# Performance work log

Hardware: AMD Instinct MI355X
Metric: run time of the kernel (lower is better)

Reference implementation:

```python
import jax, jax.numpy as jnp
import numpy as np
import math

N_LAYERS = 8
D = 1024
H = 16
DK = D // H
T = 1024
V = 32000
B = 2
DFF = 4 * D
EPS = 1e-5


def layernorm(x, scale, bias):
    mu = jnp.mean(x, axis=-1, keepdims=True)
    var = jnp.mean(jnp.square(x - mu), axis=-1, keepdims=True)
    return (x - mu) * jax.lax.rsqrt(var + EPS) * scale + bias


def setup_inputs() -> dict:
    key = jax.random.key(0)
    ks = jax.random.split(key, 32)
    s = 0.02
    rn = lambda k, shape: jax.random.normal(k, shape, dtype=jnp.float32) * s
    x = jax.random.randint(ks[0], (B, T), 0, V)
    return {
        "x": x,
        "inp_emb": rn(ks[1], (V, D)),
        "pos_emb": rn(ks[2], (T, D)),
        # per-layer weights stacked on leading layer axis; per-head wq/wk/wv are
        # concatenated along the output dim (mathematically identical to the
        # per-head nn.Linear list in the torch code)
        "wq": rn(ks[3], (N_LAYERS, D, D)), "bq": jnp.zeros((N_LAYERS, D), jnp.float32),
        "wk": rn(ks[4], (N_LAYERS, D, D)), "bk": jnp.zeros((N_LAYERS, D), jnp.float32),
        "wv": rn(ks[5], (N_LAYERS, D, D)), "bv": jnp.zeros((N_LAYERS, D), jnp.float32),
        "wo": rn(ks[6], (N_LAYERS, D, D)), "bo": jnp.zeros((N_LAYERS, D), jnp.float32),
        "w1": rn(ks[7], (N_LAYERS, D, DFF)), "b1": jnp.zeros((N_LAYERS, DFF), jnp.float32),
        "w2": rn(ks[8], (N_LAYERS, DFF, D)), "b2": jnp.zeros((N_LAYERS, D), jnp.float32),
        "ln1_s": jnp.ones((N_LAYERS, D), jnp.float32), "ln1_b": jnp.zeros((N_LAYERS, D), jnp.float32),
        "ln2_s": jnp.ones((N_LAYERS, D), jnp.float32), "ln2_b": jnp.zeros((N_LAYERS, D), jnp.float32),
        "lno_s": jnp.ones((D,), jnp.float32), "lno_b": jnp.zeros((D,), jnp.float32),
        "w_out": rn(ks[9], (D, V)),
    }


def reference(x, inp_emb, pos_emb, wq, bq, wk, bk, wv, bv, wo, bo,
              w1, b1, w2, b2, ln1_s, ln1_b, ln2_s, ln2_b, lno_s, lno_b, w_out):
    h = inp_emb[x] + pos_emb[jnp.arange(T)]            # [B,T,D]
    causal = jnp.tril(jnp.ones((T, T), dtype=bool))    # [T,T]
    scale = 1.0 / math.sqrt(DK)
    for i in range(N_LAYERS):
        # --- multi-head causal attention ---
        xn = layernorm(h, ln1_s[i], ln1_b[i])
        q = (xn @ wq[i] + bq[i]).reshape(B, T, H, DK)
        k = (xn @ wk[i] + bk[i]).reshape(B, T, H, DK)
        v = (xn @ wv[i] + bv[i]).reshape(B, T, H, DK)
        scores = jnp.einsum('bqhd,bkhd->bhqk', q, k) * scale
        scores = jnp.where(causal, scores, -jnp.inf)
        att = jax.nn.softmax(scores, axis=-1)           # [B,H,T,T]
        y = jnp.einsum('bhqk,bkhd->bqhd', att, v).reshape(B, T, D)
        h = h + y @ wo[i] + bo[i]
        # --- feed-forward ---
        xn = layernorm(h, ln2_s[i], ln2_b[i])
        h = h + jax.nn.gelu(xn @ w1[i] + b1[i], approximate=False) @ w2[i] + b2[i]
    h = layernorm(h, lno_s, lno_b)
    return h @ w_out                                    # logits [B,T,V]
```

## Files before the change

kernel.cpp:

```cpp
#include <hip/hip_runtime.h>
#include <cmath>

#define D_MODEL 1024
#define N_HEADS 16
#define DKH     64
#define SEQ_T   1024
#define BATCH   2
#define VOCAB   32000
#define DFF_    4096
#define NLAYERS 8

typedef __bf16 bf16x8 __attribute__((ext_vector_type(8)));
typedef __bf16 bf16x4v __attribute__((ext_vector_type(4)));
typedef float  f32x4  __attribute__((ext_vector_type(4)));

__device__ __forceinline__ float gelu_f(float x) {
    return 0.5f * x * (1.0f + erff(x * 0.70710678118654752f));
}

__device__ __forceinline__ void gload_lds16(const void* g, void* l) {
    __builtin_amdgcn_global_load_lds(
        (const __attribute__((address_space(1))) void*)g,
        (__attribute__((address_space(3))) void*)l, 16, 0, 0);
}

__global__ __launch_bounds__(256) void embed_kernel(
    const int* __restrict__ x, const float* __restrict__ inp_emb,
    const float* __restrict__ pos_emb, float* __restrict__ h)
{
    const int idx = blockIdx.x * 256 + threadIdx.x;
    const int bt  = idx >> 10;
    const int d   = idx & 1023;
    const int t   = bt & (SEQ_T - 1);
    const int tok = x[bt];
    h[idx] = inp_emb[(size_t)tok * D_MODEL + d] + pos_emb[(size_t)t * D_MODEL + d];
}

__device__ __forceinline__ void ln_row(
    const float* __restrict__ x, const float* __restrict__ sc,
    const float* __restrict__ bi, __bf16* __restrict__ o, int row, int tid)
{
    const int c = tid * 4;
    const float4 v = *(const float4*)(x + (size_t)row * D_MODEL + c);
    float sum = v.x + v.y + v.z + v.w;
    float sq  = v.x * v.x + v.y * v.y + v.z * v.z + v.w * v.w;
    #pragma unroll
    for (int off = 32; off > 0; off >>= 1) {
        sum += __shfl_xor(sum, off);
        sq  += __shfl_xor(sq, off);
    }
    __shared__ float ssum[4], ssq[4];
    const int wave = tid >> 6, lane = tid & 63;
    if (lane == 0) { ssum[wave] = sum; ssq[wave] = sq; }
    __syncthreads();
    sum = ssum[0] + ssum[1] + ssum[2] + ssum[3];
    sq  = ssq[0]  + ssq[1]  + ssq[2]  + ssq[3];
    const float mu  = sum * (1.0f / D_MODEL);
    const float var = sq * (1.0f / D_MODEL) - mu * mu;
    const float rs  = rsqrtf(var + 1e-5f);
    const float4 s4 = *(const float4*)(sc + c);
    const float4 b4 = *(const float4*)(bi + c);
    bf16x4v ov;
    ov[0] = (__bf16)((v.x - mu) * rs * s4.x + b4.x);
    ov[1] = (__bf16)((v.y - mu) * rs * s4.y + b4.y);
    ov[2] = (__bf16)((v.z - mu) * rs * s4.z + b4.z);
    ov[3] = (__bf16)((v.w - mu) * rs * s4.w + b4.w);
    *(bf16x4v*)(o + (size_t)row * D_MODEL + c) = ov;
}

__global__ __launch_bounds__(256) void layernorm_kernel(
    const float* __restrict__ x, const float* __restrict__ sc,
    const float* __restrict__ bi, __bf16* __restrict__ o)
{
    ln_row(x, sc, bi, o, blockIdx.x, threadIdx.x);
}

__global__ __launch_bounds__(256) void wout_tr_kernel(
    const float* __restrict__ in, __bf16* __restrict__ out)
{
    __shared__ __bf16 tile[32][72];
    const int tid = threadIdx.x;
    const int t   = blockIdx.x;
    const int kb0 = (t & 31) * 32;
    const int nb0 = (t >> 5) * 64;
    {
        const int rr = tid >> 3, c8 = (tid & 7) * 8;
        const float* p = in + (size_t)(kb0 + rr) * VOCAB + nb0 + c8;
        const float4 v0 = *(const float4*)p;
        const float4 v1 = *(const float4*)(p + 4);
        tile[rr][c8 + 0] = (__bf16)v0.x;
        tile[rr][c8 + 1] = (__bf16)v0.y;
        tile[rr][c8 + 2] = (__bf16)v0.z;
        tile[rr][c8 + 3] = (__bf16)v0.w;
        tile[rr][c8 + 4] = (__bf16)v1.x;
        tile[rr][c8 + 5] = (__bf16)v1.y;
        tile[rr][c8 + 6] = (__bf16)v1.z;
        tile[rr][c8 + 7] = (__bf16)v1.w;
    }
    __syncthreads();
    {
        const int cc = tid >> 2, k8 = (tid & 3) * 8;
        bf16x8 ov;
        #pragma unroll
        for (int e = 0; e < 8; ++e) ov[e] = tile[k8 + e][cc];
        *(bf16x8*)(out + (size_t)(nb0 + cc) * D_MODEL + kb0 + k8) = ov;
    }
}

__global__ __launch_bounds__(256) void prep_ln_kernel(
    const float* __restrict__ h, const float* __restrict__ ln_s,
    const float* __restrict__ ln_b, __bf16* __restrict__ xn,
    const float* __restrict__ wq, const float* __restrict__ wk,
    const float* __restrict__ wv, const float* __restrict__ wo,
    const float* __restrict__ w1, const float* __restrict__ w2,
    const float* __restrict__ bq, const float* __restrict__ bk,
    const float* __restrict__ bv,
    __bf16* __restrict__ wqkvT, __bf16* __restrict__ woT,
    __bf16* __restrict__ w1T, __bf16* __restrict__ w2T,
    float* __restrict__ bqkv)
{
    const int tid = threadIdx.x;
    const int b   = blockIdx.x;

    if (b < 2048) {
        ln_row(h, ln_s, ln_b, xn, b, tid);
        return;
    }
    const int pb = b - 2048;
    if (pb >= 6144) {
        const int j = (pb - 6144) * 256 + tid;
        bqkv[j] = (j < 1024) ? bq[j] : (j < 2048 ? bk[j - 1024] : bv[j - 2048]);
        return;
    }

    __shared__ __bf16 tile[32][72];
    const float* in;
    __bf16* out;
    int K, N, kb0, nb0;
    if (pb < 2048) {
        const int w = pb >> 9, t = pb & 511;
        K = 1024; N = 1024; kb0 = (t >> 4) * 32; nb0 = (t & 15) * 64;
        in  = (w == 0) ? wq : (w == 1) ? wk : (w == 2) ? wv : wo;
        out = (w == 3) ? woT : wqkvT + (size_t)w * 1024 * 1024;
    } else if (pb < 4096) {
        const int t = pb - 2048;
        K = 1024; N = 4096; kb0 = (t >> 6) * 32; nb0 = (t & 63) * 64;
        in = w1; out = w1T;
    } else {
        const int t = pb - 4096;
        K = 4096; N = 1024; kb0 = (t >> 4) * 32; nb0 = (t & 15) * 64;
        in = w2; out = w2T;
    }

    {
        const int rr = tid >> 3, c8 = (tid & 7) * 8;
        const float* p = in + (size_t)(kb0 + rr) * N + nb0 + c8;
        const float4 v0 = *(const float4*)p;
        const float4 v1 = *(const float4*)(p + 4);
        tile[rr][c8 + 0] = (__bf16)v0.x;
        tile[rr][c8 + 1] = (__bf16)v0.y;
        tile[rr][c8 + 2] = (__bf16)v0.z;
        tile[rr][c8 + 3] = (__bf16)v0.w;
        tile[rr][c8 + 4] = (__bf16)v1.x;
        tile[rr][c8 + 5] = (__bf16)v1.y;
        tile[rr][c8 + 6] = (__bf16)v1.z;
        tile[rr][c8 + 7] = (__bf16)v1.w;
    }
    __syncthreads();
    {
        const int cc = tid >> 2, k8 = (tid & 3) * 8;
        bf16x8 ov;
        #pragma unroll
        for (int e = 0; e < 8; ++e) ov[e] = tile[k8 + e][cc];
        *(bf16x8*)(out + (size_t)(nb0 + cc) * K + kb0 + k8) = ov;
    }
}

template <int BN_T, int EPI, typename OutT, bool NT = false>
__global__ __launch_bounds__(256) void gemm_bt(
    const __bf16* __restrict__ A, const __bf16* __restrict__ Bt,
    const float* __restrict__ bias, const float* __restrict__ res,
    OutT* __restrict__ C, int M, int N, int K)
{
    constexpr int NF  = BN_T / 32;
    constexpr int NCB = BN_T / 8;
    __shared__ __bf16 As[128 * 64];
    __shared__ __bf16 Bs[BN_T * 64];

    const int tid  = threadIdx.x;
    const int wave = tid >> 6;
    const int lane = tid & 63;
    const int r    = lane & 15;
    const int kb   = lane >> 4;
    const int wm   = wave >> 1;
    const int wn   = wave & 1;

    const int ntm = gridDim.x;
    const int nwg = ntm * gridDim.y;
    int bid = blockIdx.y * ntm + blockIdx.x;
    if ((nwg & 7) == 0) bid = (bid & 7) * (nwg >> 3) + (bid >> 3);
    const int bm = (bid % ntm) * 128;
    const int bn = (bid / ntm) * BN_T;

    const int srow = lane >> 3;
    const int sg   = lane & 7;

    f32x4 acc[4][NF] = {};

    for (int k0 = 0; k0 < K; k0 += 64) {
        #pragma unroll
        for (int i = 0; i < 4; ++i) {
            const int c    = i * 4 + wave;
            const int row  = c * 8 + srow;
            const int scol = (sg ^ (row & 7)) * 8;
            gload_lds16(A + (size_t)(bm + row) * K + k0 + scol, &As[c * 512]);
        }
        #pragma unroll
        for (int i = 0; i < NCB / 4; ++i) {
            const int c    = i * 4 + wave;
            const int row  = c * 8 + srow;
            const int scol = (sg ^ (row & 7)) * 8;
            gload_lds16(Bt + (size_t)(bn + row) * K + k0 + scol, &Bs[c * 512]);
        }
        __syncthreads();

        #pragma unroll
        for (int s = 0; s < 2; ++s) {
            bf16x8 af[4];
            #pragma unroll
            for (int m = 0; m < 4; ++m) {
                const int row = wm * 64 + m * 16 + r;
                const int g   = (s * 4 + kb) ^ (row & 7);
                af[m] = *(const bf16x8*)&As[row * 64 + g * 8];
            }
            #pragma unroll
            for (int n = 0; n < NF; ++n) {
                const int row = wn * (NF * 16) + n * 16 + r;
                const int g   = (s * 4 + kb) ^ (row & 7);
                const bf16x8 bfr = *(const bf16x8*)&Bs[row * 64 + g * 8];
                #pragma unroll
                for (int m = 0; m < 4; ++m)
                    acc[m][n] = __builtin_amdgcn_mfma_f32_16x16x32_bf16(af[m], bfr, acc[m][n], 0, 0, 0);
            }
        }
        __syncthreads();
    }

    #pragma unroll
    for (int m = 0; m < 4; ++m) {
        const int row = bm + wm * 64 + m * 16 + kb * 4;
        #pragma unroll
        for (int n = 0; n < NF; ++n) {
            const int col = bn + wn * (NF * 16) + n * 16 + r;
            const float bv = bias ? bias[col] : 0.0f;
            #pragma unroll
            for (int rg = 0; rg < 4; ++rg) {
                float v = acc[m][n][rg] + bv;
                if constexpr (EPI == 1) v += res[(size_t)(row + rg) * N + col];
                if constexpr (EPI == 2) v = gelu_f(v);
                if constexpr (NT) {
                    __builtin_nontemporal_store((OutT)v, &C[(size_t)(row + rg) * N + col]);
                } else {
                    C[(size_t)(row + rg) * N + col] = (OutT)v;
                }
            }
        }
    }
}

struct AttnState {
    float m[4];
    float l[4];
    f32x4 yacc[4];
};

template <bool MASK>
__device__ __forceinline__ void attn_tile_step(
    AttnState& st, const bf16x8 (&qf)[2], int q0, int kt,
    int wave, int r, int kb,
    const __bf16 (*K_lds)[72], const __bf16 (*V_lds)[72],
    __bf16 (*P_row)[72])
{
    f32x4 sacc[4] = {};
    #pragma unroll
    for (int kc = 0; kc < 2; ++kc) {
        #pragma unroll
        for (int g = 0; g < 4; ++g) {
            const bf16x8 kf = *(const bf16x8*)&K_lds[g * 16 + r][kc * 32 + kb * 8];
            sacc[g] = __builtin_amdgcn_mfma_f32_16x16x32_bf16(qf[kc], kf, sacc[g], 0, 0, 0);
        }
    }

    float s[4][4], p[4][4];
    #pragma unroll
    for (int g = 0; g < 4; ++g) {
        #pragma unroll
        for (int rg = 0; rg < 4; ++rg) {
            if constexpr (MASK) {
                const int key = kt * 64 + g * 16 + r;
                const int qq  = q0 + wave * 16 + kb * 4 + rg;
                s[g][rg] = (key <= qq) ? sacc[g][rg] * 0.125f : -INFINITY;
            } else {
                s[g][rg] = sacc[g][rg] * 0.125f;
            }
        }
    }

    float mt[4];
    #pragma unroll
    for (int rg = 0; rg < 4; ++rg)
        mt[rg] = fmaxf(fmaxf(s[0][rg], s[1][rg]), fmaxf(s[2][rg], s[3][rg]));
    #pragma unroll
    for (int off = 1; off < 16; off <<= 1) {
        #pragma unroll
        for (int rg = 0; rg < 4; ++rg) mt[rg] = fmaxf(mt[rg], __shfl_xor(mt[rg], off));
    }

    bool grow = false;
    #pragma unroll
    for (int rg = 0; rg < 4; ++rg) grow |= (mt[rg] > st.m[rg] + 8.0f);
    if (__any(grow)) {
        #pragma unroll
        for (int rg = 0; rg < 4; ++rg) {
            const float mn   = fmaxf(st.m[rg], mt[rg]);
            const float corr = __expf(st.m[rg] - mn);
            st.l[rg] *= corr;
            st.m[rg]  = mn;
            #pragma unroll
            for (int n = 0; n < 4; ++n) st.yacc[n][rg] *= corr;
        }
    }

    float psum[4];
    #pragma unroll
    for (int rg = 0; rg < 4; ++rg) {
        psum[rg] = 0.0f;
        #pragma unroll
        for (int g = 0; g < 4; ++g) {
            p[g][rg] = __expf(s[g][rg] - st.m[rg]);
            psum[rg] += p[g][rg];
        }
    }
    #pragma unroll
    for (int off = 1; off < 16; off <<= 1) {
        #pragma unroll
        for (int rg = 0; rg < 4; ++rg) psum[rg] += __shfl_xor(psum[rg], off);
    }
    #pragma unroll
    for (int rg = 0; rg < 4; ++rg) st.l[rg] += psum[rg];

    #pragma unroll
    for (int g = 0; g < 4; ++g) {
        #pragma unroll
        for (int rg = 0; rg < 4; ++rg)
            P_row[kb * 4 + rg][g * 16 + r] = (__bf16)p[g][rg];
    }
    const bf16x8 pa0 = *(const bf16x8*)&P_row[r][kb * 8];
    const bf16x8 pa1 = *(const bf16x8*)&P_row[r][32 + kb * 8];

    #pragma unroll
    for (int n = 0; n < 4; ++n) {
        const int vrow = n * 16 + r;
        const int swz  = (vrow >> 3) & 7;
        const bf16x8 vf0 = *(const bf16x8*)&V_lds[vrow][(kb ^ swz) * 8];
        st.yacc[n] = __builtin_amdgcn_mfma_f32_16x16x32_bf16(pa0, vf0, st.yacc[n], 0, 0, 0);
    }
    #pragma unroll
    for (int n = 0; n < 4; ++n) {
        const int vrow = n * 16 + r;
        const int swz  = (vrow >> 3) & 7;
        const bf16x8 vf1 = *(const bf16x8*)&V_lds[vrow][((kb + 4) ^ swz) * 8];
        st.yacc[n] = __builtin_amdgcn_mfma_f32_16x16x32_bf16(pa1, vf1, st.yacc[n], 0, 0, 0);
    }
}

__global__ __launch_bounds__(256) void attn_mfma_kernel(
    const __bf16* __restrict__ qkv, __bf16* __restrict__ y)
{
    constexpr int QS = 3 * D_MODEL;
    __shared__ __align__(16) __bf16 K_lds[64][72];
    __shared__ __align__(16) __bf16 V_lds[64][72];
    __shared__ __align__(16) __bf16 P_lds[4][16][72];

    const int tid  = threadIdx.x;
    const int wave = tid >> 6;
    const int lane = tid & 63;
    const int r    = lane & 15;
    const int kb   = lane >> 4;

    const int ip  = blockIdx.x;
    const int q0A = ip * 64;
    const int q0B = (15 - ip) * 64;
    const int b   = blockIdx.y >> 4;
    const int h   = blockIdx.y & 15;

    const __bf16* qp = qkv + (size_t)b * SEQ_T * QS + h * DKH;
    const __bf16* kp = qp + D_MODEL;
    const __bf16* vp = qp + 2 * D_MODEL;
    __bf16* yp = y + (size_t)b * SEQ_T * D_MODEL + h * DKH;

    bf16x8 qfA[2], qfB[2];
    {
        const int qrA = q0A + wave * 16 + r;
        const int qrB = q0B + wave * 16 + r;
        #pragma unroll
        for (int kc = 0; kc < 2; ++kc) {
            qfA[kc] = *(const bf16x8*)(qp + (size_t)qrA * QS + kc * 32 + kb * 8);
            qfB[kc] = *(const bf16x8*)(qp + (size_t)qrB * QS + kc * 32 + kb * 8);
        }
    }

    AttnState stA, stB;
    #pragma unroll
    for (int rg = 0; rg < 4; ++rg) {
        stA.m[rg] = -INFINITY; stA.l[rg] = 0.0f;
        stB.m[rg] = -INFINITY; stB.l[rg] = 0.0f;
    }
    #pragma unroll
    for (int n = 0; n < 4; ++n) { stA.yacc[n] = {}; stB.yacc[n] = {}; }

    const int skey = tid >> 2;
    const int sg16 = (tid & 3) * 16;
    const int swz0 = ((sg16 >> 3) & 7) * 8;
    const int swz1 = (((sg16 + 8) >> 3) & 7) * 8;

    const int ntiles = 16 - ip;

    bf16x8 kr0, kr1, vr0, vr1;
    {
        const size_t go = (size_t)skey * QS;
        kr0 = *(const bf16x8*)(kp + go + sg16);
        kr1 = *(const bf16x8*)(kp + go + sg16 + 8);
        vr0 = *(const bf16x8*)(vp + go + sg16);
        vr1 = *(const bf16x8*)(vp + go + sg16 + 8);
    }

    for (int kt = 0; kt < ntiles; ++kt) {
        *(bf16x8*)&K_lds[skey][sg16]     = kr0;
        *(bf16x8*)&K_lds[skey][sg16 + 8] = kr1;
        #pragma unroll
        for (int j = 0; j < 8; ++j)
            V_lds[sg16 + j][skey ^ swz0] = vr0[j];
        #pragma unroll
        for (int j = 0; j < 8; ++j)
            V_lds[sg16 + 8 + j][skey ^ swz1] = vr1[j];
        __syncthreads();

        if (kt + 1 < ntiles) {
            const size_t go = (size_t)((kt + 1) * 64 + skey) * QS;
            kr0 = *(const bf16x8*)(kp + go + sg16);
            kr1 = *(const bf16x8*)(kp + go + sg16 + 8);
            vr0 = *(const bf16x8*)(vp + go + sg16);
            vr1 = *(const bf16x8*)(vp + go + sg16 + 8);
        }

        if (kt == ntiles - 1)
            attn_tile_step<true >(stB, qfB, q0B, kt, wave, r, kb, K_lds, V_lds, P_lds[wave]);
        else
            attn_tile_step<false>(stB, qfB, q0B, kt, wave, r, kb, K_lds, V_lds, P_lds[wave]);
        if (kt <= ip) {
            if (kt == ip)
                attn_tile_step<true >(stA, qfA, q0A, kt, wave, r, kb, K_lds, V_lds, P_lds[wave]);
            else
                attn_tile_step<false>(stA, qfA, q0A, kt, wave, r, kb, K_lds, V_lds, P_lds[wave]);
        }
        __syncthreads();
    }

    float invA[4], invB[4];
    #pragma unroll
    for (int rg = 0; rg < 4; ++rg) {
        invA[rg] = 1.0f / stA.l[rg];
        invB[rg] = 1.0f / stB.l[rg];
    }
    #pragma unroll
    for (int n = 0; n < 4; ++n) {
        #pragma unroll
        for (int rg = 0; rg < 4; ++rg) {
            const int rowA = q0A + wave * 16 + kb * 4 + rg;
            const int rowB = q0B + wave * 16 + kb * 4 + rg;
            yp[(size_t)rowA * D_MODEL + n * 16 + r] = (__bf16)(stA.yacc[n][rg] * invA[rg]);
            yp[(size_t)rowB * D_MODEL + n * 16 + r] = (__bf16)(stB.yacc[n][rg] * invB[rg]);
        }
    }
}

extern "C" void kernel_launch(void* const* d_in, const int* in_sizes, int n_in,
                              void* d_out, int out_size, void* d_ws, size_t ws_size,
                              hipStream_t stream)
{
    const int*   x       = (const int*)  d_in[0];
    const float* inp_emb = (const float*)d_in[1];
    const float* pos_emb = (const float*)d_in[2];
    const float* wq = (const float*)d_in[3];
    const float* bq = (const float*)d_in[4];
    const float* wk = (const float*)d_in[5];
    const float* bk = (const float*)d_in[6];
    const float* wv = (const float*)d_in[7];
    const float* bv = (const float*)d_in[8];
    const float* wo = (const float*)d_in[9];
    const float* bo = (const float*)d_in[10];
    const float* w1 = (const float*)d_in[11];
    const float* b1 = (const float*)d_in[12];
    const float* w2 = (const float*)d_in[13];
    const float* b2 = (const float*)d_in[14];
    const float* ln1_s = (const float*)d_in[15];
    const float* ln1_b = (const float*)d_in[16];
    const float* ln2_s = (const float*)d_in[17];
    const float* ln2_b = (const float*)d_in[18];
    const float* lno_s = (const float*)d_in[19];
    const float* lno_b = (const float*)d_in[20];
    const float* w_out = (const float*)d_in[21];

    const int M = BATCH * SEQ_T;
    const size_t MB = 1u << 20;

    char* w = (char*)d_ws;
    float*  h     = (float*) (w + 0);
    __bf16* xn    = (__bf16*)(w + 8  * MB);
    __bf16* yb    = (__bf16*)(w + 12 * MB);
    __bf16* sh    = (__bf16*)(w + 16 * MB);
    __bf16* wqkvT = (__bf16*)(w + 32 * MB);
    __bf16* woT   = (__bf16*)(w + 38 * MB);
    __bf16* w1T   = (__bf16*)(w + 40 * MB);
    __bf16* w2T   = (__bf16*)(w + 48 * MB);
    float*  bqkv  = (float*) (w + 56 * MB);
    __bf16* woutT = (__bf16*)(w + 57 * MB);

    embed_kernel<<<dim3(M * D_MODEL / 256), 256, 0, stream>>>(x, inp_emb, pos_emb, h);

    for (int i = 0; i < NLAYERS; ++i) {
        const size_t wOff  = (size_t)i * D_MODEL * D_MODEL;
        const size_t w1Off = (size_t)i * D_MODEL * DFF_;

        prep_ln_kernel<<<dim3(2048 + 6156), 256, 0, stream>>>(
            h, ln1_s + i * D_MODEL, ln1_b + i * D_MODEL, xn,
            wq + wOff, wk + wOff, wv + wOff, wo + wOff, w1 + w1Off, w2 + w1Off,
            bq + i * D_MODEL, bk + i * D_MODEL, bv + i * D_MODEL,
            wqkvT, woT, w1T, w2T, bqkv);

        gemm_bt<64, 0, __bf16><<<dim3(M / 128, 3 * D_MODEL / 64), 256, 0, stream>>>(
            xn, wqkvT, bqkv, nullptr, sh, M, 3 * D_MODEL, D_MODEL);
        attn_mfma_kernel<<<dim3(8, BATCH * N_HEADS), 256, 0, stream>>>(sh, yb);
        gemm_bt<64, 1, float><<<dim3(M / 128, D_MODEL / 64), 256, 0, stream>>>(
            yb, woT, bo + i * D_MODEL, h, h, M, D_MODEL, D_MODEL);
        layernorm_kernel<<<dim3(M), 256, 0, stream>>>(h, ln2_s + i * D_MODEL, ln2_b + i * D_MODEL, xn);
        gemm_bt<128, 2, __bf16><<<dim3(M / 128, DFF_ / 128), 256, 0, stream>>>(
            xn, w1T, b1 + i * DFF_, nullptr, sh, M, DFF_, D_MODEL);
        gemm_bt<64, 1, float><<<dim3(M / 128, D_MODEL / 64), 256, 0, stream>>>(
            sh, w2T, b2 + i * D_MODEL, h, h, M, D_MODEL, DFF_);
    }

    wout_tr_kernel<<<dim3(16000), 256, 0, stream>>>(w_out, woutT);
    layernorm_kernel<<<dim3(M), 256, 0, stream>>>(h, lno_s, lno_b, xn);
    gemm_bt<128, 0, float, true><<<dim3(M / 128, VOCAB / 128), 256, 0, stream>>>(
        xn, woutT, nullptr, nullptr, (float*)d_out, M, VOCAB, D_MODEL);
}
```

Baseline: 1.631 ms.

## Store residual stream in bf16, double-buffer attention K/V, fuse final LN

```diff
diff --git a/kernel.cpp b/kernel.cpp
--- a/kernel.cpp
+++ b/kernel.cpp
@@ -26,24 +26,32 @@
 
 __global__ __launch_bounds__(256) void embed_kernel(
     const int* __restrict__ x, const float* __restrict__ inp_emb,
-    const float* __restrict__ pos_emb, float* __restrict__ h)
-{
-    const int idx = blockIdx.x * 256 + threadIdx.x;
+    const float* __restrict__ pos_emb, __bf16* __restrict__ h)
+{
+    const int idx = (blockIdx.x * 256 + threadIdx.x) * 4;
     const int bt  = idx >> 10;
     const int d   = idx & 1023;
     const int t   = bt & (SEQ_T - 1);
     const int tok = x[bt];
-    h[idx] = inp_emb[(size_t)tok * D_MODEL + d] + pos_emb[(size_t)t * D_MODEL + d];
+    const float4 a = *(const float4*)(inp_emb + (size_t)tok * D_MODEL + d);
+    const float4 b = *(const float4*)(pos_emb + (size_t)t * D_MODEL + d);
+    bf16x4v o;
+    o[0] = (__bf16)(a.x + b.x);
+    o[1] = (__bf16)(a.y + b.y);
+    o[2] = (__bf16)(a.z + b.z);
+    o[3] = (__bf16)(a.w + b.w);
+    *(bf16x4v*)(h + idx) = o;
 }
 
 __device__ __forceinline__ void ln_row(
-    const float* __restrict__ x, const float* __restrict__ sc,
+    const __bf16* __restrict__ x, const float* __restrict__ sc,
     const float* __restrict__ bi, __bf16* __restrict__ o, int row, int tid)
 {
     const int c = tid * 4;
-    const float4 v = *(const float4*)(x + (size_t)row * D_MODEL + c);
-    float sum = v.x + v.y + v.z + v.w;
-    float sq  = v.x * v.x + v.y * v.y + v.z * v.z + v.w * v.w;
+    const bf16x4v v4 = *(const bf16x4v*)(x + (size_t)row * D_MODEL + c);
+    const float vx = (float)v4[0], vy = (float)v4[1], vz = (float)v4[2], vw = (float)v4[3];
+    float sum = vx + vy + vz + vw;
+    float sq  = vx * vx + vy * vy + vz * vz + vw * vw;
     #pragma unroll
     for (int off = 32; off > 0; off >>= 1) {
         sum += __shfl_xor(sum, off);
@@ -61,25 +69,31 @@
     const float4 s4 = *(const float4*)(sc + c);
     const float4 b4 = *(const float4*)(bi + c);
     bf16x4v ov;
-    ov[0] = (__bf16)((v.x - mu) * rs * s4.x + b4.x);
-    ov[1] = (__bf16)((v.y - mu) * rs * s4.y + b4.y);
-    ov[2] = (__bf16)((v.z - mu) * rs * s4.z + b4.z);
-    ov[3] = (__bf16)((v.w - mu) * rs * s4.w + b4.w);
+    ov[0] = (__bf16)((vx - mu) * rs * s4.x + b4.x);
+    ov[1] = (__bf16)((vy - mu) * rs * s4.y + b4.y);
+    ov[2] = (__bf16)((vz - mu) * rs * s4.z + b4.z);
+    ov[3] = (__bf16)((vw - mu) * rs * s4.w + b4.w);
     *(bf16x4v*)(o + (size_t)row * D_MODEL + c) = ov;
 }
 
 __global__ __launch_bounds__(256) void layernorm_kernel(
-    const float* __restrict__ x, const float* __restrict__ sc,
+    const __bf16* __restrict__ x, const float* __restrict__ sc,
     const float* __restrict__ bi, __bf16* __restrict__ o)
 {
     ln_row(x, sc, bi, o, blockIdx.x, threadIdx.x);
 }
 
-__global__ __launch_bounds__(256) void wout_tr_kernel(
-    const float* __restrict__ in, __bf16* __restrict__ out)
-{
+__global__ __launch_bounds__(256) void wout_ln_kernel(
+    const float* __restrict__ in, __bf16* __restrict__ out,
+    const __bf16* __restrict__ h, const float* __restrict__ lno_s,
+    const float* __restrict__ lno_b, __bf16* __restrict__ xn)
+{
+    const int tid = threadIdx.x;
+    if (blockIdx.x >= 16000) {
+        ln_row(h, lno_s, lno_b, xn, blockIdx.x - 16000, tid);
+        return;
+    }
     __shared__ __bf16 tile[32][72];
-    const int tid = threadIdx.x;
     const int t   = blockIdx.x;
     const int kb0 = (t & 31) * 32;
     const int nb0 = (t >> 5) * 64;
@@ -108,7 +122,7 @@
 }
 
 __global__ __launch_bounds__(256) void prep_ln_kernel(
-    const float* __restrict__ h, const float* __restrict__ ln_s,
+    const __bf16* __restrict__ h, const float* __restrict__ ln_s,
     const float* __restrict__ ln_b, __bf16* __restrict__ xn,
     const float* __restrict__ wq, const float* __restrict__ wk,
     const float* __restrict__ wv, const float* __restrict__ wo,
@@ -179,7 +193,7 @@
 template <int BN_T, int EPI, typename OutT, bool NT = false>
 __global__ __launch_bounds__(256) void gemm_bt(
     const __bf16* __restrict__ A, const __bf16* __restrict__ Bt,
-    const float* __restrict__ bias, const float* __restrict__ res,
+    const float* __restrict__ bias, const OutT* __restrict__ res,
     OutT* __restrict__ C, int M, int N, int K)
 {
     constexpr int NF  = BN_T / 32;
@@ -256,7 +270,7 @@
             #pragma unroll
             for (int rg = 0; rg < 4; ++rg) {
                 float v = acc[m][n][rg] + bv;
-                if constexpr (EPI == 1) v += res[(size_t)(row + rg) * N + col];
+                if constexpr (EPI == 1) v += (float)res[(size_t)(row + rg) * N + col];
                 if constexpr (EPI == 2) v = gelu_f(v);
                 if constexpr (NT) {
                     __builtin_nontemporal_store((OutT)v, &C[(size_t)(row + rg) * N + col]);
@@ -378,8 +392,8 @@
     const __bf16* __restrict__ qkv, __bf16* __restrict__ y)
 {
     constexpr int QS = 3 * D_MODEL;
-    __shared__ __align__(16) __bf16 K_lds[64][72];
-    __shared__ __align__(16) __bf16 V_lds[64][72];
+    __shared__ __align__(16) __bf16 K_lds[2][64][72];
+    __shared__ __align__(16) __bf16 V_lds[2][64][72];
     __shared__ __align__(16) __bf16 P_lds[4][16][72];
 
     const int tid  = threadIdx.x;
@@ -434,19 +448,18 @@
         vr0 = *(const bf16x8*)(vp + go + sg16);
         vr1 = *(const bf16x8*)(vp + go + sg16 + 8);
     }
-
+    *(bf16x8*)&K_lds[0][skey][sg16]     = kr0;
+    *(bf16x8*)&K_lds[0][skey][sg16 + 8] = kr1;
+    #pragma unroll
+    for (int j = 0; j < 8; ++j) V_lds[0][sg16 + j][skey ^ swz0]     = vr0[j];
+    #pragma unroll
+    for (int j = 0; j < 8; ++j) V_lds[0][sg16 + 8 + j][skey ^ swz1] = vr1[j];
+    __syncthreads();
+
+    int cur = 0;
     for (int kt = 0; kt < ntiles; ++kt) {
-        *(bf16x8*)&K_lds[skey][sg16]     = kr0;
-        *(bf16x8*)&K_lds[skey][sg16 + 8] = kr1;
-        #pragma unroll
-        for (int j = 0; j < 8; ++j)
-            V_lds[sg16 + j][skey ^ swz0] = vr0[j];
-        #pragma unroll
-        for (int j = 0; j < 8; ++j)
-            V_lds[sg16 + 8 + j][skey ^ swz1] = vr1[j];
-        __syncthreads();
-
-        if (kt + 1 < ntiles) {
+        const bool has_next = (kt + 1 < ntiles);
+        if (has_next) {
             const size_t go = (size_t)((kt + 1) * 64 + skey) * QS;
             kr0 = *(const bf16x8*)(kp + go + sg16);
             kr1 = *(const bf16x8*)(kp + go + sg16 + 8);
@@ -455,16 +468,27 @@
         }
 
         if (kt == ntiles - 1)
-            attn_tile_step<true >(stB, qfB, q0B, kt, wave, r, kb, K_lds, V_lds, P_lds[wave]);
+            attn_tile_step<true >(stB, qfB, q0B, kt, wave, r, kb, K_lds[cur], V_lds[cur], P_lds[wave]);
         else
-            attn_tile_step<false>(stB, qfB, q0B, kt, wave, r, kb, K_lds, V_lds, P_lds[wave]);
+            attn_tile_step<false>(stB, qfB, q0B, kt, wave, r, kb, K_lds[cur], V_lds[cur], P_lds[wave]);
         if (kt <= ip) {
             if (kt == ip)
-                attn_tile_step<true >(stA, qfA, q0A, kt, wave, r, kb, K_lds, V_lds, P_lds[wave]);
+                attn_tile_step<true >(stA, qfA, q0A, kt, wave, r, kb, K_lds[cur], V_lds[cur], P_lds[wave]);
             else
-                attn_tile_step<false>(stA, qfA, q0A, kt, wave, r, kb, K_lds, V_lds, P_lds[wave]);
+                attn_tile_step<false>(stA, qfA, q0A, kt, wave, r, kb, K_lds[cur], V_lds[cur], P_lds[wave]);
+        }
+
+        if (has_next) {
+            const int nb = cur ^ 1;
+            *(bf16x8*)&K_lds[nb][skey][sg16]     = kr0;
+            *(bf16x8*)&K_lds[nb][skey][sg16 + 8] = kr1;
+            #pragma unroll
+            for (int j = 0; j < 8; ++j) V_lds[nb][sg16 + j][skey ^ swz0]     = vr0[j];
+            #pragma unroll
+            for (int j = 0; j < 8; ++j) V_lds[nb][sg16 + 8 + j][skey ^ swz1] = vr1[j];
         }
         __syncthreads();
+        cur ^= 1;
     }
 
     float invA[4], invB[4];
@@ -516,7 +540,7 @@
     const size_t MB = 1u << 20;
 
     char* w = (char*)d_ws;
-    float*  h     = (float*) (w + 0);
+    __bf16* h     = (__bf16*)(w + 0);
     __bf16* xn    = (__bf16*)(w + 8  * MB);
     __bf16* yb    = (__bf16*)(w + 12 * MB);
     __bf16* sh    = (__bf16*)(w + 16 * MB);
@@ -527,7 +551,7 @@
     float*  bqkv  = (float*) (w + 56 * MB);
     __bf16* woutT = (__bf16*)(w + 57 * MB);
 
-    embed_kernel<<<dim3(M * D_MODEL / 256), 256, 0, stream>>>(x, inp_emb, pos_emb, h);
+    embed_kernel<<<dim3(M * D_MODEL / 1024), 256, 0, stream>>>(x, inp_emb, pos_emb, h);
 
     for (int i = 0; i < NLAYERS; ++i) {
         const size_t wOff  = (size_t)i * D_MODEL * D_MODEL;
@@ -542,17 +566,17 @@
         gemm_bt<64, 0, __bf16><<<dim3(M / 128, 3 * D_MODEL / 64), 256, 0, stream>>>(
             xn, wqkvT, bqkv, nullptr, sh, M, 3 * D_MODEL, D_MODEL);
         attn_mfma_kernel<<<dim3(8, BATCH * N_HEADS), 256, 0, stream>>>(sh, yb);
-        gemm_bt<64, 1, float><<<dim3(M / 128, D_MODEL / 64), 256, 0, stream>>>(
+        gemm_bt<64, 1, __bf16><<<dim3(M / 128, D_MODEL / 64), 256, 0, stream>>>(
             yb, woT, bo + i * D_MODEL, h, h, M, D_MODEL, D_MODEL);
         layernorm_kernel<<<dim3(M), 256, 0, stream>>>(h, ln2_s + i * D_MODEL, ln2_b + i * D_MODEL, xn);
         gemm_bt<128, 2, __bf16><<<dim3(M / 128, DFF_ / 128), 256, 0, stream>>>(
             xn, w1T, b1 + i * DFF_, nullptr, sh, M, DFF_, D_MODEL);
-        gemm_bt<64, 1, float><<<dim3(M / 128, D_MODEL / 64), 256, 0, stream>>>(
+        gemm_bt<64, 1, __bf16><<<dim3(M / 128, D_MODEL / 64), 256, 0, stream>>>(
             sh, w2T, b2 + i * D_MODEL, h, h, M, D_MODEL, DFF_);
     }
 
-    wout_tr_kernel<<<dim3(16000), 256, 0, stream>>>(w_out, woutT);
-    layernorm_kernel<<<dim3(M), 256, 0, stream>>>(h, lno_s, lno_b, xn);
+    wout_ln_kernel<<<dim3(16000 + 2048), 256, 0, stream>>>(
+        w_out, woutT, h, lno_s, lno_b, xn);
     gemm_bt<128, 0, float, true><<<dim3(M / 128, VOCAB / 128), 256, 0, stream>>>(
         xn, woutT, nullptr, nullptr, (float*)d_out, M, VOCAB, D_MODEL);
 }
```

Measured after the change: 1.652 ms. Within noise of the previous version (+1.3%).
